# Optimization experiments

Hardware: AMD Instinct MI355X
Metric: run time of the kernel (lower is better)

## Reference

```python
import jax, jax.numpy as jnp
import numpy as np

HIDDEN = 1024
NH = 4
DK = 1024          # key_dim = hidden * expand_k
DV = 2048          # value_dim = hidden * expand_v
HDK = DK // NH     # 256
HDV = DV // NH     # 512
LOWRANK = 16
GATE_NORM = 16.0
CHUNK = 64
EPS = 1e-5


def setup_inputs() -> dict:
    key = jax.random.key(0)
    ks = jax.random.split(key, 10)
    s = 0.02  # xavier-ish init scale (gain 2**-2.5)
    return {
        "hidden_states": jax.random.normal(ks[0], (4, 2048, HIDDEN), dtype=jnp.float32),
        "Wq": jax.random.normal(ks[1], (HIDDEN, DK), dtype=jnp.float32) * s,
        "Wk": jax.random.normal(ks[2], (HIDDEN, DK), dtype=jnp.float32) * s,
        "Wv": jax.random.normal(ks[3], (HIDDEN, DV), dtype=jnp.float32) * s,
        "Wg": jax.random.normal(ks[4], (HIDDEN, DV), dtype=jnp.float32) * s,
        "Wgk1": jax.random.normal(ks[5], (HIDDEN, LOWRANK), dtype=jnp.float32) * s,
        "Wgk2": jax.random.normal(ks[6], (LOWRANK, DK), dtype=jnp.float32) * s,
        "bgk2": jnp.zeros((DK,), dtype=jnp.float32),
        "g_norm_w": jnp.ones((HDV,), dtype=jnp.float32),
        "Wo": jax.random.normal(ks[7], (DV, HIDDEN), dtype=jnp.float32) * s,
    }


def _gla_chunked(q, k, v, gk):
    """Chunked gated linear attention.
    q, k, gk: [B, H, L, dk]; v: [B, H, L, dv]. Recurrence:
      S_t = diag(exp(gk_t)) S_{t-1} + k_t^T v_t ; o_t = (q_t * scale) S_t
    """
    B, H, L, dk = q.shape
    dv = v.shape[-1]
    N = L // CHUNK
    scale = dk ** -0.5

    def split(x):  # [B,H,L,d] -> [N,B,H,C,d]
        x = x.reshape(B, H, N, CHUNK, x.shape[-1])
        return jnp.moveaxis(x, 2, 0)

    qc, kc, vc, gc = split(q), split(k), split(v), split(gk)
    mask = jnp.tril(jnp.ones((CHUNK, CHUNK), dtype=bool))

    def step(S, inp):
        q_c, k_c, v_c, g_c = inp                 # [B,H,C,dk] / [B,H,C,dv]
        b = jnp.cumsum(g_c, axis=2)              # inclusive cumulative log-decay
        b_last = b[:, :, -1:, :]                 # [B,H,1,dk]
        q_g = q_c * jnp.exp(b) * scale           # decayed queries
        k_intra = k_c * jnp.exp(-b)              # for intra-chunk scores
        k_state = k_c * jnp.exp(b_last - b)      # for state update
        # intra-chunk causal scores: s_ij = q_i k_j exp(b_i - b_j), j <= i
        scores = jnp.einsum('bhid,bhjd->bhij', q_g, k_intra)
        scores = jnp.where(mask, scores, 0.0)
        o_intra = jnp.einsum('bhij,bhjv->bhiv', scores, v_c)
        o_inter = jnp.einsum('bhid,bhdv->bhiv', q_g, S)
        S_new = S * jnp.exp(b_last[:, :, 0, :])[..., None] \
            + jnp.einsum('bhcd,bhcv->bhdv', k_state, v_c)
        return S_new, o_intra + o_inter

    S0 = jnp.zeros((B, H, dk, dv), dtype=q.dtype)
    _, o = jax.lax.scan(step, S0, (qc, kc, vc, gc))
    o = jnp.moveaxis(o, 0, 2).reshape(B, H, L, dv)
    return o


def reference(hidden_states, Wq, Wk, Wv, Wg, Wgk1, Wgk2, bgk2, g_norm_w, Wo):
    B, L, _ = hidden_states.shape
    h = hidden_states

    def heads(x, hd):  # [B,L,H*hd] -> [B,H,L,hd]
        return x.reshape(B, L, NH, hd).transpose(0, 2, 1, 3)

    q = heads(h @ Wq, HDK)
    k = heads(h @ Wk, HDK)
    v = heads(h @ Wv, HDV)
    gk_raw = (h @ Wgk1) @ Wgk2 + bgk2
    gk = jax.nn.log_sigmoid(gk_raw) / GATE_NORM
    gk = heads(gk, HDK)

    o = _gla_chunked(q, k, v, gk)                # [B,H,L,hdv]
    o = o.transpose(0, 2, 1, 3)                  # [B,L,H,hdv]

    # FusedRMSNormSwishGate: rmsnorm(o) * silu(g), per head_v_dim
    g = (h @ Wg).reshape(B, L, NH, HDV)
    rms = o * jax.lax.rsqrt(jnp.mean(o * o, axis=-1, keepdims=True) + EPS)
    o = rms * g_norm_w * (g * jax.nn.sigmoid(g))
    o = o.reshape(B, L, DV)
    return o @ Wo
```

## Files before the change

kernel.cpp:

```cpp
#include <hip/hip_runtime.h>
#include <stdint.h>


typedef float f32x4 __attribute__((ext_vector_type(4)));
typedef short s16x8 __attribute__((ext_vector_type(8)));
typedef short s16x4 __attribute__((ext_vector_type(4)));

#define DEVINL __device__ __forceinline__

DEVINL short f2bf(float f) {
  union { float f; uint32_t u; } v; v.f = f;
  uint32_t r = v.u + 0x7fffu + ((v.u >> 16) & 1u);
  return (short)(r >> 16);
}
DEVINL float bf2f(short s) {
  union { uint32_t u; float f; } v; v.u = ((uint32_t)(uint16_t)s) << 16;
  return v.f;
}
DEVINL f32x4 mfma16(s16x8 a, s16x8 b, f32x4 c) {
  return __builtin_amdgcn_mfma_f32_16x16x32_bf16(a, b, c, 0, 0, 0);
}
#define ASYNC_COPY16(G, L)                                                   \
  __builtin_amdgcn_global_load_lds(                                          \
      (__attribute__((address_space(1))) void*)(void*)(G),                   \
      (__attribute__((address_space(3))) void*)(L), 16, 0, 0)

__global__ __launch_bounds__(256) void cvt_f2b_vec(const float* __restrict__ src,
                                                   short* __restrict__ dst) {
  int id = blockIdx.x * 256 + threadIdx.x;
  f32x4 v = ((const f32x4*)src)[id];
  s16x4 o = { f2bf(v[0]), f2bf(v[1]), f2bf(v[2]), f2bf(v[3]) };
  ((s16x4*)dst)[id] = o;
}

__global__ __launch_bounds__(256) void transpose_weights(
    const float* __restrict__ Wq, const float* __restrict__ Wk,
    const float* __restrict__ Wv, const float* __restrict__ Wg,
    const float* __restrict__ Wo, short* __restrict__ wT,
    short* __restrict__ woT) {
  __shared__ short sh[64 * 66];
  const float* src; short* dst; int K, N;
  switch (blockIdx.z) {
    case 0: src = Wq; dst = wT;                         K = 1024; N = 1024; break;
    case 1: src = Wk; dst = wT + (size_t)1024 * 1024;   K = 1024; N = 1024; break;
    case 2: src = Wv; dst = wT + (size_t)2048 * 1024;   K = 1024; N = 2048; break;
    case 3: src = Wg; dst = wT + (size_t)4096 * 1024;   K = 1024; N = 2048; break;
    default: src = Wo; dst = woT;                       K = 2048; N = 1024; break;
  }
  int n0 = blockIdx.x * 64, k0 = blockIdx.y * 64;
  if (n0 >= N || k0 >= K) return;
  int tx = threadIdx.x & 63, ty = threadIdx.x >> 6;
#pragma unroll
  for (int j = 0; j < 16; j++) {
    int r = j * 4 + ty;
    sh[r * 66 + tx] = f2bf(src[(size_t)(k0 + r) * N + n0 + tx]);
  }
  __syncthreads();
#pragma unroll
  for (int j = 0; j < 16; j++) {
    int r = j * 4 + ty;
    dst[(size_t)(n0 + r) * K + k0 + tx] = sh[tx * 66 + r];
  }
}

__global__ __launch_bounds__(256) void transpose_s16_batched(const short* __restrict__ src,
                                                             short* __restrict__ dst,
                                                             int K, int N) {
  __shared__ short sh[64 * 66];
  size_t boff = (size_t)blockIdx.z * K * N;
  int n0 = blockIdx.x * 64, k0 = blockIdx.y * 64;
  int tx = threadIdx.x & 63, ty = threadIdx.x >> 6;
#pragma unroll
  for (int j = 0; j < 16; j++) {
    int r = j * 4 + ty;
    sh[r * 66 + tx] = src[boff + (size_t)(k0 + r) * N + n0 + tx];
  }
  __syncthreads();
#pragma unroll
  for (int j = 0; j < 16; j++) {
    int r = j * 4 + ty;
    dst[boff + (size_t)(n0 + r) * K + k0 + tx] = sh[tx * 66 + r];
  }
}

__global__ __launch_bounds__(256) void gk_fused(const float* __restrict__ h,
                                                const float* __restrict__ W1,
                                                const float* __restrict__ W2,
                                                const float* __restrict__ b2,
                                                float* __restrict__ gk) {
  __shared__ float pbuf[32][8][16];
  __shared__ float hl[32][16];
  const int tid = threadIdx.x;
  const int tok0 = blockIdx.x * 32;
  {
    const int tok = tid >> 3, kg = tid & 7;
    const float* hrow = h + (size_t)(tok0 + tok) * 1024 + kg * 128;
    float p[16];
#pragma unroll
    for (int c = 0; c < 16; c++) p[c] = 0.f;
    for (int i = 0; i < 128; i++) {
      float hv = hrow[i];
      const float* wrow = W1 + (size_t)(kg * 128 + i) * 16;
#pragma unroll
      for (int c = 0; c < 16; c++) p[c] += hv * wrow[c];
    }
#pragma unroll
    for (int c = 0; c < 16; c++) pbuf[tok][kg][c] = p[c];
  }
  __syncthreads();
  for (int o = tid; o < 512; o += 256) {
    int tok = o >> 4, c = o & 15;
    float s = 0.f;
#pragma unroll
    for (int g = 0; g < 8; g++) s += pbuf[tok][g][c];
    hl[tok][c] = s;
  }
  __syncthreads();
#pragma unroll
  for (int j = 0; j < 4; j++) {
    int n = j * 256 + tid;
    float w[16];
#pragma unroll
    for (int c = 0; c < 16; c++) w[c] = W2[c * 1024 + n];
    float bias = b2[n];
    for (int t = 0; t < 32; t++) {
      float raw = bias;
#pragma unroll
      for (int c = 0; c < 16; c++) raw += hl[t][c] * w[c];
      float ls = fminf(raw, 0.f) - log1pf(__expf(-fabsf(raw)));
      gk[(size_t)(tok0 + t) * 1024 + n] = ls * 0.0625f;
    }
  }
}

template <int MODE>
__global__ __launch_bounds__(256) void gemm_bf16(const short* __restrict__ A,
                                                 const short* __restrict__ Bt, int K,
                                                 short* __restrict__ oQ,
                                                 short* __restrict__ oK,
                                                 short* __restrict__ oV,
                                                 short* __restrict__ oG,
                                                 float* __restrict__ oD) {
  __shared__ short ldsA[128 * 64];
  __shared__ short ldsB[128 * 64];
  const int tid = threadIdx.x;
  const int w = tid >> 6, lane = tid & 63;
  const int wm = w >> 1, wn = w & 1;
  int bx, by;
  {
    const int orig = blockIdx.y * gridDim.x + blockIdx.x;
    const int x = orig & 7;
    const int j = orig >> 3;
    if (MODE == 0) {
      const int rx = x & 3, ry = x >> 2;
      const int sub = j >> 6, t = j & 63;
      const int sx = sub & 1, sy = sub >> 1;
      bx = rx * 16 + sx * 8 + (t & 7);
      by = ry * 24 + sy * 8 + (t >> 3);
    } else {
      bx = x * 8 + (j & 7);
      by = j >> 3;
    }
  }
  const int rowA0 = bx * 128, rowB0 = by * 128;
  f32x4 acc[4][4];
#pragma unroll
  for (int m = 0; m < 4; m++)
#pragma unroll
    for (int n = 0; n < 4; n++) acc[m][n] = (f32x4){0.f, 0.f, 0.f, 0.f};

  for (int kt = 0; kt < K; kt += 64) {
#pragma unroll
    for (int i = 0; i < 4; i++) {
      int X = i * 4096 + tid * 16;
      int r = X >> 7;
      int cB = (X & 127) ^ ((r & 7) << 4);
      ASYNC_COPY16((const char*)A + ((size_t)(rowA0 + r) * K + kt) * 2 + cB,
                   (char*)ldsA + X);
      ASYNC_COPY16((const char*)Bt + ((size_t)(rowB0 + r) * K + kt) * 2 + cB,
                   (char*)ldsB + X);
    }
    __syncthreads();
#pragma unroll
    for (int kk = 0; kk < 2; kk++) {
      s16x8 af[4], bfv[4];
#pragma unroll
      for (int mt = 0; mt < 4; mt++) {
        int row = wm * 64 + mt * 16 + (lane & 15);
        int lin = row * 128 + (kk * 32 + 8 * (lane >> 4)) * 2;
        af[mt] = *(const s16x8*)((const char*)ldsA + (lin ^ ((row & 7) << 4)));
      }
#pragma unroll
      for (int nt = 0; nt < 4; nt++) {
        int rowb = wn * 64 + nt * 16 + (lane & 15);
        int lin = rowb * 128 + (kk * 32 + 8 * (lane >> 4)) * 2;
        bfv[nt] = *(const s16x8*)((const char*)ldsB + (lin ^ ((rowb & 7) << 4)));
      }
#pragma unroll
      for (int mt = 0; mt < 4; mt++)
#pragma unroll
        for (int nt = 0; nt < 4; nt++) acc[mt][nt] = mfma16(af[mt], bfv[nt], acc[mt][nt]);
    }
    __syncthreads();
  }
#pragma unroll
  for (int mt = 0; mt < 4; mt++) {
#pragma unroll
    for (int nt = 0; nt < 4; nt++) {
      int grow0 = rowA0 + wm * 64 + mt * 16 + 4 * (lane >> 4);
      int gcol = rowB0 + wn * 64 + nt * 16 + (lane & 15);
#pragma unroll
      for (int r = 0; r < 4; r++) {
        int grow = grow0 + r;
        float val = acc[mt][nt][r];
        if (MODE == 0) {
          int sec = gcol >> 10;
          if (sec == 0)      oQ[(size_t)grow * 1024 + gcol] = f2bf(val);
          else if (sec == 1) oK[(size_t)grow * 1024 + (gcol - 1024)] = f2bf(val);
          else if (sec < 4)  oV[(size_t)grow * 2048 + (gcol - 2048)] = f2bf(val);
          else               oG[(size_t)grow * 2048 + (gcol - 4096)] = f2bf(val);
        } else {
          oD[(size_t)grow * 1024 + gcol] = val;
        }
      }
    }
  }
}

__global__ __launch_bounds__(256) void gla_intra(const short* __restrict__ Qb,
                                                 const short* __restrict__ Kb,
                                                 const float* __restrict__ gkp,
                                                 const short* __restrict__ VbT,
                                                 short* __restrict__ qg_g,
                                                 short* __restrict__ ksT_g,
                                                 float* __restrict__ Adec,
                                                 short* __restrict__ obA) {
  __shared__ short smem[64 * 512];
  __shared__ short scorebuf[64 * 64];
  __shared__ float adecs[256];
  short* qgbuf = smem;
  short* kibuf = smem + 64 * 256;

  const int ch = blockIdx.x, bh = blockIdx.y;
  const int b = bh >> 2, h = bh & 3;
  const int tok0 = b * 2048 + ch * 64;
  const int ltk0 = ch * 64;
  const int tid = threadIdx.x;
  const int col = h * 256 + tid;

  const float scale_ = 0.0625f;
  float cs = 0.f;
#pragma unroll 4
  for (int t = 0; t < 64; t++) {
    size_t ri = (size_t)(tok0 + t) * 1024 + col;
    cs += gkp[ri];
    float qv = bf2f(Qb[ri]);
    float kv = bf2f(Kb[ri]);
    float ep = __expf(cs);
    float en = __expf(-cs);
    short qb = f2bf(qv * ep * scale_);
    short kb = f2bf(kv * en);
    int lin = t * 512 + tid * 2;
    int sw = (t & 7) << 4;
    *(short*)((char*)qgbuf + (lin ^ sw)) = qb;
    *(short*)((char*)kibuf + (lin ^ sw)) = kb;
    qg_g[ri] = qb;
  }
  float elast = __expf(cs);
  Adec[(bh * 32 + ch) * 256 + tid] = elast;
  adecs[tid] = elast;
  __syncthreads();

  const int w = tid >> 6, lane = tid & 63;
  {
    f32x4 sc[4];
#pragma unroll
    for (int nt = 0; nt < 4; nt++) sc[nt] = (f32x4){0.f, 0.f, 0.f, 0.f};
#pragma unroll
    for (int kk = 0; kk < 8; kk++) {
      int row = 16 * w + (lane & 15);
      int lin = row * 512 + (kk * 32 + 8 * (lane >> 4)) * 2;
      s16x8 a = *(const s16x8*)((const char*)qgbuf + (lin ^ ((row & 7) << 4)));
#pragma unroll
      for (int nt = 0; nt < 4; nt++) {
        int tj = nt * 16 + (lane & 15);
        int linb = tj * 512 + (kk * 32 + 8 * (lane >> 4)) * 2;
        s16x8 bb = *(const s16x8*)((const char*)kibuf + (linb ^ ((tj & 7) << 4)));
        sc[nt] = mfma16(a, bb, sc[nt]);
      }
    }
#pragma unroll
    for (int nt = 0; nt < 4; nt++) {
#pragma unroll
      for (int r = 0; r < 4; r++) {
        int ri = 16 * w + 4 * (lane >> 4) + r;
        int cj = nt * 16 + (lane & 15);
        float v = (cj <= ri) ? sc[nt][r] : 0.f;
        int lin = ri * 128 + cj * 2;
        *(short*)((char*)scorebuf + (lin ^ ((ri & 7) << 4))) = f2bf(v);
      }
    }
  }
  __syncthreads();

  size_t ksb = (size_t)(bh * 32 + ch) * 16384;
#pragma unroll
  for (int j = 0; j < 8; j++) {
    int E = j * 2048 + tid * 8;
    int d = E >> 6, t0 = E & 63;
    float el = adecs[d];
    s16x8 v;
#pragma unroll
    for (int r = 0; r < 8; r++) {
      int t = t0 + r;
      short ki = *(const short*)((const char*)kibuf + ((t * 512 + d * 2) ^ ((t & 7) << 4)));
      v[r] = f2bf(bf2f(ki) * el);
    }
    *(s16x8*)(ksT_g + ksb + E) = v;
  }
  __syncthreads();

  {
    s16x8 a2[2];
#pragma unroll
    for (int kk = 0; kk < 2; kk++) {
      int row = 16 * w + (lane & 15);
      int lin = row * 128 + (kk * 32 + 8 * (lane >> 4)) * 2;
      a2[kk] = *(const s16x8*)((const char*)scorebuf + (lin ^ ((row & 7) << 4)));
    }
    for (int nt = 0; nt < 32; nt++) {
      int e = nt * 16 + (lane & 15);
      f32x4 oacc = (f32x4){0.f, 0.f, 0.f, 0.f};
#pragma unroll
      for (int kk = 0; kk < 2; kk++) {
        const s16x8 bb = *(const s16x8*)(VbT + ((size_t)bh * 512 + e) * 2048 + ltk0 + kk * 32 + 8 * (lane >> 4));
        oacc = mfma16(a2[kk], bb, oacc);
      }
#pragma unroll
      for (int r = 0; r < 4; r++) {
        int ri = 16 * w + 4 * (lane >> 4) + r;
        int lin3 = ri * 1024 + e * 2;
        *(short*)((char*)smem + (lin3 ^ ((ri & 7) << 4))) = f2bf(oacc[r]);
      }
    }
  }
  __syncthreads();
#pragma unroll
  for (int it = 0; it < 16; it++) {
    int row = it * 4 + (tid >> 6);
    int vec = tid & 63;
    int lin = row * 1024 + vec * 16;
    s16x8 v = *(const s16x8*)((const char*)smem + (lin ^ ((row & 7) << 4)));
    *(s16x8*)(obA + (size_t)(tok0 + row) * 2048 + h * 512 + vec * 8) = v;
  }
}

__global__ __launch_bounds__(256) void gla_state(const short* __restrict__ ksT_g,
                                                 const short* __restrict__ VbT,
                                                 const float* __restrict__ Adec,
                                                 short* __restrict__ Sb) {
  __shared__ short st[32 * 256];
  const int seg = blockIdx.x, bh = blockIdx.y;
  const int tid = threadIdx.x;
  const int w = tid >> 6, lane = tid & 63;

  f32x4 S[4][2];
#pragma unroll
  for (int mt = 0; mt < 4; mt++)
#pragma unroll
    for (int nt = 0; nt < 2; nt++) S[mt][nt] = (f32x4){0.f, 0.f, 0.f, 0.f};

  for (int ch = 0; ch < 24; ch++) {
    const int ltk0 = ch * 64;
#pragma unroll
    for (int mt = 0; mt < 4; mt++) {
      int dkb = 64 * w + mt * 16 + 4 * (lane >> 4);
      f32x4 a = *(const f32x4*)(Adec + (size_t)(bh * 32 + ch) * 256 + dkb);
#pragma unroll
      for (int nt = 0; nt < 2; nt++) {
        S[mt][nt][0] *= a[0]; S[mt][nt][1] *= a[1];
        S[mt][nt][2] *= a[2]; S[mt][nt][3] *= a[3];
      }
    }
    size_t ksb = (size_t)(bh * 32 + ch) * 16384;
#pragma unroll
    for (int kk = 0; kk < 2; kk++) {
      s16x8 ak[4];
#pragma unroll
      for (int mt = 0; mt < 4; mt++) {
        int dk = 64 * w + mt * 16 + (lane & 15);
        ak[mt] = *(const s16x8*)(ksT_g + ksb + (size_t)dk * 64 + kk * 32 + 8 * (lane >> 4));
      }
#pragma unroll
      for (int nt = 0; nt < 2; nt++) {
        int e = seg * 32 + nt * 16 + (lane & 15);
        s16x8 bv = *(const s16x8*)(VbT + ((size_t)bh * 512 + e) * 2048 + ltk0 + kk * 32 + 8 * (lane >> 4));
#pragma unroll
        for (int mt = 0; mt < 4; mt++) S[mt][nt] = mfma16(ak[mt], bv, S[mt][nt]);
      }
    }
    if (ch == 7 || ch == 15 || ch == 23) {
      int g = (ch - 7) >> 3;
      __syncthreads();
#pragma unroll
      for (int mt = 0; mt < 4; mt++) {
#pragma unroll
        for (int nt = 0; nt < 2; nt++) {
          int dv = nt * 16 + (lane & 15);
          int dk0 = 64 * w + mt * 16 + 4 * (lane >> 4);
          s16x4 pk = { f2bf(S[mt][nt][0]), f2bf(S[mt][nt][1]), f2bf(S[mt][nt][2]), f2bf(S[mt][nt][3]) };
          int lin = dv * 512 + dk0 * 2;
          *(s16x4*)((char*)st + (lin ^ ((dv & 7) << 4))) = pk;
        }
      }
      __syncthreads();
      char* dstb = (char*)Sb + (((size_t)(g * 16 + bh) * 512 + seg * 32) * 256) * 2;
#pragma unroll
      for (int it = 0; it < 4; it++) {
        int dv = it * 8 + (tid >> 5);
        int vec = tid & 31;
        int X = dv * 512 + vec * 16;
        s16x8 v = *(const s16x8*)((const char*)st + (X ^ ((dv & 7) << 4)));
        *(s16x8*)(dstb + X) = v;
      }
    }
  }
}

__global__ __launch_bounds__(512) void gla_scan(const short* __restrict__ qg_g,
                                                const short* __restrict__ ksT_g,
                                                const short* __restrict__ VbT,
                                                const float* __restrict__ Adec,
                                                const short* __restrict__ Sb,
                                                short* __restrict__ obB) {
  __shared__ short st[32 * 256];
  const int seg = blockIdx.x, bh = blockIdx.y, gz = blockIdx.z;
  const int b = bh >> 2, h = bh & 3;
  const int tid = threadIdx.x;
  const int w = tid >> 6, lane = tid & 63;
  const int tt = w & 3;
  const int dh = w >> 2;
  const int ch0 = gz * 8;

  f32x4 S[2][2];
#pragma unroll
  for (int mt = 0; mt < 2; mt++)
#pragma unroll
    for (int nt = 0; nt < 2; nt++) S[mt][nt] = (f32x4){0.f, 0.f, 0.f, 0.f};

  if (gz > 0) {
    const char* srcb = (const char*)Sb + ((((size_t)(gz - 1) * 16 + bh) * 512 + seg * 32) * 256) * 2;
#pragma unroll
    for (int it = 0; it < 2; it++) {
      int dv = it * 16 + (tid >> 5);
      int vec = tid & 31;
      int X = dv * 512 + vec * 16;
      s16x8 v = *(const s16x8*)(srcb + X);
      *(s16x8*)((char*)st + (X ^ ((dv & 7) << 4))) = v;
    }
    __syncthreads();
#pragma unroll
    for (int mt = 0; mt < 2; mt++) {
#pragma unroll
      for (int nt = 0; nt < 2; nt++) {
        int dv = nt * 16 + (lane & 15);
        int dk0 = 32 * w + mt * 16 + 4 * (lane >> 4);
        int lin = dv * 512 + dk0 * 2;
        s16x4 pk = *(const s16x4*)((const char*)st + (lin ^ ((dv & 7) << 4)));
        S[mt][nt][0] = bf2f(pk[0]); S[mt][nt][1] = bf2f(pk[1]);
        S[mt][nt][2] = bf2f(pk[2]); S[mt][nt][3] = bf2f(pk[3]);
      }
    }
  }

  for (int ch = ch0; ch < ch0 + 8; ch++) {
    const int tok0 = b * 2048 + ch * 64;
    const int ltk0 = ch * 64;

    if (ch != ch0 || gz == 0) {
#pragma unroll
      for (int mt = 0; mt < 2; mt++) {
#pragma unroll
        for (int nt = 0; nt < 2; nt++) {
          int dv = nt * 16 + (lane & 15);
          int dk0 = 32 * w + mt * 16 + 4 * (lane >> 4);
          s16x4 pk = { f2bf(S[mt][nt][0]), f2bf(S[mt][nt][1]), f2bf(S[mt][nt][2]), f2bf(S[mt][nt][3]) };
          int lin = dv * 512 + dk0 * 2;
          *(s16x4*)((char*)st + (lin ^ ((dv & 7) << 4))) = pk;
        }
      }
    }
    __syncthreads();

    {
      s16x8 aq[8];
#pragma unroll
      for (int kk = 0; kk < 8; kk++) {
        int ti = tok0 + 16 * tt + (lane & 15);
        aq[kk] = *(const s16x8*)(qg_g + (size_t)ti * 1024 + h * 256 + kk * 32 + 8 * (lane >> 4));
      }
      f32x4 oi0 = (f32x4){0.f, 0.f, 0.f, 0.f};
      f32x4 oi1 = (f32x4){0.f, 0.f, 0.f, 0.f};
      int dv = 16 * dh + (lane & 15);
      __builtin_amdgcn_s_setprio(1);
#pragma unroll
      for (int kk = 0; kk < 8; kk += 2) {
        int lin0 = dv * 512 + (kk * 32 + 8 * (lane >> 4)) * 2;
        int lin1 = dv * 512 + ((kk + 1) * 32 + 8 * (lane >> 4)) * 2;
        s16x8 b0 = *(const s16x8*)((const char*)st + (lin0 ^ ((dv & 7) << 4)));
        s16x8 b1 = *(const s16x8*)((const char*)st + (lin1 ^ ((dv & 7) << 4)));
        oi0 = mfma16(aq[kk], b0, oi0);
        oi1 = mfma16(aq[kk + 1], b1, oi1);
      }
      __builtin_amdgcn_s_setprio(0);
#pragma unroll
      for (int r = 0; r < 4; r++) {
        int ti = tok0 + 16 * tt + 4 * (lane >> 4) + r;
        obB[(size_t)ti * 2048 + h * 512 + seg * 32 + 16 * dh + (lane & 15)] =
            f2bf(oi0[r] + oi1[r]);
      }
    }

#pragma unroll
    for (int mt = 0; mt < 2; mt++) {
      int dkb = 32 * w + mt * 16 + 4 * (lane >> 4);
      f32x4 a = *(const f32x4*)(Adec + (size_t)(bh * 32 + ch) * 256 + dkb);
#pragma unroll
      for (int nt = 0; nt < 2; nt++) {
        S[mt][nt][0] *= a[0]; S[mt][nt][1] *= a[1];
        S[mt][nt][2] *= a[2]; S[mt][nt][3] *= a[3];
      }
    }

    size_t ksb = (size_t)(bh * 32 + ch) * 16384;
#pragma unroll
    for (int kk = 0; kk < 2; kk++) {
      s16x8 ak[2];
#pragma unroll
      for (int mt = 0; mt < 2; mt++) {
        int dk = 32 * w + mt * 16 + (lane & 15);
        ak[mt] = *(const s16x8*)(ksT_g + ksb + (size_t)dk * 64 + kk * 32 + 8 * (lane >> 4));
      }
#pragma unroll
      for (int nt = 0; nt < 2; nt++) {
        int e = seg * 32 + nt * 16 + (lane & 15);
        s16x8 bv = *(const s16x8*)(VbT + ((size_t)bh * 512 + e) * 2048 + ltk0 + kk * 32 + 8 * (lane >> 4));
#pragma unroll
        for (int mt = 0; mt < 2; mt++) S[mt][nt] = mfma16(ak[mt], bv, S[mt][nt]);
      }
    }
    __syncthreads();
  }
}

__global__ __launch_bounds__(256) void gate_norm(const short* __restrict__ obA,
                                                 const short* __restrict__ obB,
                                                 const short* __restrict__ Gb,
                                                 const float* __restrict__ gnw,
                                                 short* __restrict__ gated) {
  int row = blockIdx.x, tid = threadIdx.x;
  int lane = tid & 63;
  size_t base = (size_t)row * 2048 + (tid >> 6) * 512 + lane * 8;
  s16x8 av = *(const s16x8*)(obA + base);
  s16x8 bv = *(const s16x8*)(obB + base);
  s16x8 gv = *(const s16x8*)(Gb + base);
  float o[8];
  float ss = 0.f;
#pragma unroll
  for (int j = 0; j < 8; j++) {
    o[j] = bf2f(av[j]) + bf2f(bv[j]);
    ss += o[j] * o[j];
  }
#pragma unroll
  for (int off = 32; off > 0; off >>= 1) ss += __shfl_xor(ss, off);
  float rinv = rsqrtf(ss * (1.0f / 512.0f) + 1e-5f);
  f32x4 w0 = *(const f32x4*)(gnw + lane * 8);
  f32x4 w1 = *(const f32x4*)(gnw + lane * 8 + 4);
  s16x8 out;
#pragma unroll
  for (int j = 0; j < 8; j++) {
    float g = bf2f(gv[j]);
    float sg = g / (1.f + __expf(-g));
    float wj = (j < 4) ? w0[j] : w1[j - 4];
    out[j] = f2bf(o[j] * rinv * wj * sg);
  }
  *(s16x8*)(gated + base) = out;
}

extern "C" void kernel_launch(void* const* d_in, const int* in_sizes, int n_in,
                              void* d_out, int out_size, void* d_ws, size_t ws_size,
                              hipStream_t stream) {
  const float* hsrc = (const float*)d_in[0];
  const float* Wq   = (const float*)d_in[1];
  const float* Wk   = (const float*)d_in[2];
  const float* Wv   = (const float*)d_in[3];
  const float* Wg   = (const float*)d_in[4];
  const float* Wgk1 = (const float*)d_in[5];
  const float* Wgk2 = (const float*)d_in[6];
  const float* bgk2 = (const float*)d_in[7];
  const float* gnw  = (const float*)d_in[8];
  const float* Wo   = (const float*)d_in[9];
  float* out = (float*)d_out;

  short* hbf = (short*)d_ws;
  short* wT  = hbf + (size_t)8192 * 1024;
  short* woT = wT + (size_t)6144 * 1024;
  short* Qb  = woT + (size_t)1024 * 2048;
  short* Kb  = Qb + (size_t)8192 * 1024;
  short* Vb  = Kb + (size_t)8192 * 1024;
  short* Gb  = Vb + (size_t)8192 * 2048;
  short* VbT = Gb + (size_t)8192 * 2048;
  short* ksT = VbT + (size_t)8192 * 2048;
  short* obA = ksT + (size_t)16 * 32 * 256 * 64;
  float* gkb = (float*)(obA + (size_t)8192 * 2048);
  float* Adec = gkb + (size_t)8192 * 1024;
  short* Sb  = (short*)(Adec + (size_t)16 * 32 * 256);
  short* qg    = hbf;
  short* gated = Vb;
  short* obB   = (short*)d_out;

  cvt_f2b_vec<<<8192, 256, 0, stream>>>(hsrc, hbf);
  transpose_weights<<<dim3(32, 32, 5), 256, 0, stream>>>(Wq, Wk, Wv, Wg, Wo, wT, woT);
  gk_fused<<<256, 256, 0, stream>>>(hsrc, Wgk1, Wgk2, bgk2, gkb);
  gemm_bf16<0><<<dim3(64, 48), 256, 0, stream>>>(hbf, wT, 1024, Qb, Kb, Vb, Gb, nullptr);
  transpose_s16_batched<<<dim3(32, 32, 4), 256, 0, stream>>>(Vb, VbT, 2048, 2048);
  gla_intra<<<dim3(32, 16), 256, 0, stream>>>(Qb, Kb, gkb, VbT, qg, ksT, Adec, obA);
  gla_state<<<dim3(16, 16), 256, 0, stream>>>(ksT, VbT, Adec, Sb);
  gla_scan<<<dim3(16, 16, 4), 512, 0, stream>>>(qg, ksT, VbT, Adec, Sb, obB);
  gate_norm<<<8192, 256, 0, stream>>>(obA, obB, Gb, gnw, gated);
  gemm_bf16<1><<<dim3(64, 8), 256, 0, stream>>>(gated, woT, 2048, nullptr, nullptr, nullptr, nullptr, out);
}
```

Baseline: 656.6 us.

## Replace projection GEMM with 256x256 double-buffered async-pipelined kernel

The fused QKVG projection GEMM moves from 128x128 tiles with 4 waves and a single LDS buffer to 256x256 tiles with 8 waves. The new kernel double-buffers LDS, using explicit vmcnt waits to prefetch the next K slice while the current one is computed, and raises wave priority around the MFMA bursts. The goal is more operand reuse per byte loaded and hiding global-load latency behind compute. In exchange it drops the block-swizzle used for L2 locality, uses 128KB of LDS and many accumulator registers, and launches only 768 blocks, which can reduce occupancy and leave a partial last wave. The output GEMM is split into its own non-swizzled kernel.

```diff
diff --git a/kernel.cpp b/kernel.cpp
--- a/kernel.cpp
+++ b/kernel.cpp
@@ -133,36 +133,112 @@
   }
 }
 
-template <int MODE>
-__global__ __launch_bounds__(256) void gemm_bf16(const short* __restrict__ A,
-                                                 const short* __restrict__ Bt, int K,
-                                                 short* __restrict__ oQ,
-                                                 short* __restrict__ oK,
-                                                 short* __restrict__ oV,
-                                                 short* __restrict__ oG,
-                                                 float* __restrict__ oD) {
+__global__ __launch_bounds__(512, 2) void gemm256(const short* __restrict__ A,
+                                                  const short* __restrict__ Bt, int K,
+                                                  short* __restrict__ oQ,
+                                                  short* __restrict__ oK,
+                                                  short* __restrict__ oV,
+                                                  short* __restrict__ oG) {
+  __shared__ short lds[2][2][2][128 * 64];
+  const int tid = threadIdx.x;
+  const int wv = tid >> 6, lane = tid & 63;
+  const int wm = wv >> 2, wn = wv & 3;
+  const int rowA0 = blockIdx.x * 256, rowB0 = blockIdx.y * 256;
+  const int NT = K >> 6;
+
+  f32x4 acc[8][4];
+#pragma unroll
+  for (int i = 0; i < 8; i++)
+#pragma unroll
+    for (int j = 0; j < 4; j++) acc[i][j] = (f32x4){0.f, 0.f, 0.f, 0.f};
+
+#define STAGE256(kt, buf)                                                          \
+  do {                                                                             \
+    _Pragma("unroll") for (int part = 0; part < 2; part++) {                       \
+      int X = part * 8192 + tid * 16;                                              \
+      int r = X >> 7;                                                              \
+      int cB = (X & 127) ^ ((r & 7) << 4);                                         \
+      _Pragma("unroll") for (int half = 0; half < 2; half++) {                     \
+        ASYNC_COPY16((const char*)A + ((size_t)(rowA0 + half * 128 + r) * K + (kt)) * 2 + cB, \
+                     (char*)&lds[buf][0][half][0] + X);                            \
+        ASYNC_COPY16((const char*)Bt + ((size_t)(rowB0 + half * 128 + r) * K + (kt)) * 2 + cB, \
+                     (char*)&lds[buf][1][half][0] + X);                            \
+      }                                                                            \
+    }                                                                              \
+  } while (0)
+
+  STAGE256(0, 0);
+  if (NT > 1) STAGE256(64, 1);
+
+  for (int t = 0; t < NT; t++) {
+    const int cur = t & 1;
+    if (t + 1 < NT) asm volatile("s_waitcnt vmcnt(8)" ::: "memory");
+    else            asm volatile("s_waitcnt vmcnt(0)" ::: "memory");
+    __builtin_amdgcn_s_barrier();
+    __builtin_amdgcn_sched_barrier(0);
+#pragma unroll
+    for (int kk = 0; kk < 2; kk++) {
+      s16x8 af[8];
+#pragma unroll
+      for (int rt = 0; rt < 8; rt++) {
+        int lr = rt * 16 + (lane & 15);
+        int lin = lr * 128 + (kk * 32 + 8 * (lane >> 4)) * 2;
+        af[rt] = *(const s16x8*)((const char*)&lds[cur][0][wm][0] + (lin ^ ((lr & 7) << 4)));
+      }
+#pragma unroll
+      for (int ch = 0; ch < 2; ch++) {
+        s16x8 bf[2];
+#pragma unroll
+        for (int ct = 0; ct < 2; ct++) {
+          int col = wn * 64 + ch * 32 + ct * 16 + (lane & 15);
+          int bh = col >> 7, lc = col & 127;
+          int lin = lc * 128 + (kk * 32 + 8 * (lane >> 4)) * 2;
+          bf[ct] = *(const s16x8*)((const char*)&lds[cur][1][bh][0] + (lin ^ ((lc & 7) << 4)));
+        }
+        __builtin_amdgcn_s_setprio(1);
+#pragma unroll
+        for (int rt = 0; rt < 8; rt++) {
+          acc[rt][ch * 2 + 0] = mfma16(af[rt], bf[0], acc[rt][ch * 2 + 0]);
+          acc[rt][ch * 2 + 1] = mfma16(af[rt], bf[1], acc[rt][ch * 2 + 1]);
+        }
+        __builtin_amdgcn_s_setprio(0);
+      }
+    }
+    __builtin_amdgcn_sched_barrier(0);
+    __builtin_amdgcn_s_barrier();
+    if (t + 2 < NT) STAGE256((t + 2) * 64, cur);
+  }
+
+#pragma unroll
+  for (int rt = 0; rt < 8; rt++) {
+#pragma unroll
+    for (int ct = 0; ct < 4; ct++) {
+      int grow0 = rowA0 + wm * 128 + rt * 16 + 4 * (lane >> 4);
+      int gcol = rowB0 + wn * 64 + ct * 16 + (lane & 15);
+      int sec = gcol >> 10;
+#pragma unroll
+      for (int r = 0; r < 4; r++) {
+        int grow = grow0 + r;
+        float val = acc[rt][ct][r];
+        if (sec == 0)      oQ[(size_t)grow * 1024 + gcol] = f2bf(val);
+        else if (sec == 1) oK[(size_t)grow * 1024 + (gcol - 1024)] = f2bf(val);
+        else if (sec < 4)  oV[(size_t)grow * 2048 + (gcol - 2048)] = f2bf(val);
+        else               oG[(size_t)grow * 2048 + (gcol - 4096)] = f2bf(val);
+      }
+    }
+  }
+#undef STAGE256
+}
+
+__global__ __launch_bounds__(256) void gemm_out(const short* __restrict__ A,
+                                                const short* __restrict__ Bt, int K,
+                                                float* __restrict__ oD) {
   __shared__ short ldsA[128 * 64];
   __shared__ short ldsB[128 * 64];
   const int tid = threadIdx.x;
   const int w = tid >> 6, lane = tid & 63;
   const int wm = w >> 1, wn = w & 1;
-  int bx, by;
-  {
-    const int orig = blockIdx.y * gridDim.x + blockIdx.x;
-    const int x = orig & 7;
-    const int j = orig >> 3;
-    if (MODE == 0) {
-      const int rx = x & 3, ry = x >> 2;
-      const int sub = j >> 6, t = j & 63;
-      const int sx = sub & 1, sy = sub >> 1;
-      bx = rx * 16 + sx * 8 + (t & 7);
-      by = ry * 24 + sy * 8 + (t >> 3);
-    } else {
-      bx = x * 8 + (j & 7);
-      by = j >> 3;
-    }
-  }
-  const int rowA0 = bx * 128, rowB0 = by * 128;
+  const int rowA0 = blockIdx.x * 128, rowB0 = blockIdx.y * 128;
   f32x4 acc[4][4];
 #pragma unroll
   for (int m = 0; m < 4; m++)
@@ -211,17 +287,7 @@
       int gcol = rowB0 + wn * 64 + nt * 16 + (lane & 15);
 #pragma unroll
       for (int r = 0; r < 4; r++) {
-        int grow = grow0 + r;
-        float val = acc[mt][nt][r];
-        if (MODE == 0) {
-          int sec = gcol >> 10;
-          if (sec == 0)      oQ[(size_t)grow * 1024 + gcol] = f2bf(val);
-          else if (sec == 1) oK[(size_t)grow * 1024 + (gcol - 1024)] = f2bf(val);
-          else if (sec < 4)  oV[(size_t)grow * 2048 + (gcol - 2048)] = f2bf(val);
-          else               oG[(size_t)grow * 2048 + (gcol - 4096)] = f2bf(val);
-        } else {
-          oD[(size_t)grow * 1024 + gcol] = val;
-        }
+        oD[(size_t)(grow0 + r) * 1024 + gcol] = acc[mt][nt][r];
       }
     }
   }
@@ -622,11 +688,11 @@
   cvt_f2b_vec<<<8192, 256, 0, stream>>>(hsrc, hbf);
   transpose_weights<<<dim3(32, 32, 5), 256, 0, stream>>>(Wq, Wk, Wv, Wg, Wo, wT, woT);
   gk_fused<<<256, 256, 0, stream>>>(hsrc, Wgk1, Wgk2, bgk2, gkb);
-  gemm_bf16<0><<<dim3(64, 48), 256, 0, stream>>>(hbf, wT, 1024, Qb, Kb, Vb, Gb, nullptr);
+  gemm256<<<dim3(32, 24), 512, 0, stream>>>(hbf, wT, 1024, Qb, Kb, Vb, Gb);
   transpose_s16_batched<<<dim3(32, 32, 4), 256, 0, stream>>>(Vb, VbT, 2048, 2048);
   gla_intra<<<dim3(32, 16), 256, 0, stream>>>(Qb, Kb, gkb, VbT, qg, ksT, Adec, obA);
   gla_state<<<dim3(16, 16), 256, 0, stream>>>(ksT, VbT, Adec, Sb);
   gla_scan<<<dim3(16, 16, 4), 512, 0, stream>>>(qg, ksT, VbT, Adec, Sb, obB);
   gate_norm<<<8192, 256, 0, stream>>>(obA, obB, Gb, gnw, gated);
-  gemm_bf16<1><<<dim3(64, 8), 256, 0, stream>>>(gated, woT, 2048, nullptr, nullptr, nullptr, nullptr, out);
-}
+  gemm_out<<<dim3(64, 8), 256, 0, stream>>>(gated, woT, 2048, out);
+}
```

Result: no change. 652.4 us (-0.6%).
